# Kernel optimization log

Measured on AMD Instinct MI355X. Metric: run time of the kernel, lower is better.

The kernel has to match this reference:

```python
import jax, jax.numpy as jnp
import numpy as np

E, D, H1, H2, O, B = 100, 2048, 512, 256, 1, 1024


def setup_inputs() -> dict:
    key = jax.random.key(0)
    ks = jax.random.split(key, 7)
    s = lambda k, shape, fan_in: jax.random.normal(k, shape, jnp.float32) * (1.0 / np.sqrt(fan_in))
    return {
        "x": jax.random.normal(ks[0], (B, D), jnp.float32),
        "W1": s(ks[1], (E, D, H1), D),
        "b1": jnp.zeros((E, H1), jnp.float32),
        "W2": s(ks[2], (E, H1, H2), H1),
        "b2": jnp.zeros((E, H2), jnp.float32),
        "W3": s(ks[3], (E, H2, O), H2),
        "b3": jnp.zeros((E, O), jnp.float32),
    }


def reference(x, W1, b1, W2, b2, W3, b3):
    # Ensemble of E independent 3-layer MLPs, expressed as batched GEMMs
    # over the ensemble axis (equivalent to the torch loop + stack(dim=2)).
    h = jax.nn.relu(jnp.einsum('bd,edh->ebh', x, W1) + b1[:, None, :])   # [E,B,H1]
    h = jax.nn.relu(jnp.einsum('ebh,ehk->ebk', h, W2) + b2[:, None, :])  # [E,B,H2]
    out = jnp.einsum('ebk,eko->ebo', h, W3) + b3[:, None, :]             # [E,B,O]
    # torch.stack([...], dim=2): each model output [B,O] -> [B,O,E]
    return jnp.transpose(out, (1, 2, 0))
```

## Files before the change

### kernel.cpp

```cpp
#include <hip/hip_runtime.h>
#include <hip/hip_bf16.h>
#include <cstdint>
#include <cstddef>

#define E_  100
#define D_  2048
#define H1_ 512
#define H2_ 256
#define B_  1024

typedef __bf16 bf16x8 __attribute__((ext_vector_type(8)));
typedef float  f32x4  __attribute__((ext_vector_type(4)));

typedef __attribute__((address_space(1))) void gvoid;
typedef __attribute__((address_space(3))) void lvoid;

__device__ __forceinline__ unsigned short f2bf(float f){
    union { float f; unsigned int u; } x; x.f = f;
    unsigned int r = x.u + 0x7fffu + ((x.u >> 16) & 1u);
    return (unsigned short)(r >> 16);
}
__device__ __forceinline__ float bf2f(unsigned int u){
    union { unsigned int i; float f; } x; x.i = u << 16; return x.f;
}

__global__ __launch_bounds__(256) void cvt_x_kernel(const float* __restrict__ x,
                                                    unsigned short* __restrict__ xb){
    int i = blockIdx.x * 256 + threadIdx.x;
    float4 v = ((const float4*)x)[i];
    ushort4 o;
    o.x = f2bf(v.x); o.y = f2bf(v.y); o.z = f2bf(v.z); o.w = f2bf(v.w);
    ((ushort4*)xb)[i] = o;
}

__global__ __launch_bounds__(256) void transpose_cvt_kernel(const float* __restrict__ src,
                                                            unsigned short* __restrict__ dst,
                                                            int R, int C){
    __shared__ unsigned int T[64 * 32];
    const int e  = blockIdx.z;
    const int r0 = blockIdx.y * 64, c0 = blockIdx.x * 64;
    const float* s = src + (size_t)e * R * C;
    unsigned short* d = dst + (size_t)e * R * C;
    const int t  = threadIdx.x;
    const int c4 = (t & 15) * 4;
    #pragma unroll
    for (int pass = 0; pass < 2; ++pass){
        const int rp = (t >> 4) + pass * 16;
        const int r  = rp * 2;
        const float4 va = *(const float4*)(s + (size_t)(r0 + r)     * C + c0 + c4);
        const float4 vb = *(const float4*)(s + (size_t)(r0 + r + 1) * C + c0 + c4);
        const float aa[4] = {va.x, va.y, va.z, va.w};
        const float bb[4] = {vb.x, vb.y, vb.z, vb.w};
        #pragma unroll
        for (int i = 0; i < 4; ++i){
            const int c = c4 + i;
            const unsigned int pk = (unsigned int)f2bf(aa[i]) | ((unsigned int)f2bf(bb[i]) << 16);
            T[c * 32 + (rp ^ (c & 31))] = pk;
        }
    }
    __syncthreads();
    const int c  = t >> 2;
    const int j0 = (t & 3) * 8;
    unsigned int tmp[8];
    #pragma unroll
    for (int j = 0; j < 8; ++j)
        tmp[j] = T[c * 32 + ((j0 + j) ^ (c & 31))];
    unsigned short* drow = d + (size_t)(c0 + c) * R + r0 + j0 * 2;
    ((uint4*)drow)[0] = make_uint4(tmp[0], tmp[1], tmp[2], tmp[3]);
    ((uint4*)drow)[1] = make_uint4(tmp[4], tmp[5], tmp[6], tmp[7]);
}

__global__ __launch_bounds__(256) void gemm_bt_relu(const unsigned short* __restrict__ A,
                                                    long long aEstride,
                                                    const unsigned short* __restrict__ Bt,
                                                    const float* __restrict__ bias,
                                                    unsigned short* __restrict__ Cout,
                                                    int M, int N, int K){
    __shared__ unsigned short As[128 * 32];
    __shared__ unsigned short Bs[128 * 32];
    const int e  = blockIdx.z;
    const int m0 = blockIdx.y * 128, n0 = blockIdx.x * 128;
    const int t = threadIdx.x, lane = t & 63, wid = t >> 6;
    const int wm = wid >> 1, wn = wid & 1;

    const unsigned short* Ae = A + (size_t)e * (size_t)aEstride + (size_t)m0 * K;
    const unsigned short* Be = Bt + (size_t)e * (size_t)N * K + (size_t)n0 * K;

    const int ch0 = wid * 128 + lane;
    const int r0s = ch0 >> 2, k0s = (((ch0 & 3) ^ ((ch0 >> 3) & 3)) * 8);
    const int ch1 = ch0 + 64;
    const int r1s = ch1 >> 2, k1s = (((ch1 & 3) ^ ((ch1 >> 3) & 3)) * 8);

    f32x4 acc[4][4];
    #pragma unroll
    for (int i = 0; i < 4; ++i)
        #pragma unroll
        for (int j = 0; j < 4; ++j) acc[i][j] = 0;

    const int fr  = lane & 15;
    const int fc  = lane >> 4;
    const int fsw = (fr >> 1) & 3;
    const int fo  = ((fc ^ fsw) * 8);

    for (int k0 = 0; k0 < K; k0 += 32){
        __builtin_amdgcn_global_load_lds((gvoid*)(Ae + (size_t)r0s * K + k0 + k0s),
                                         (lvoid*)(As + (wid * 2 + 0) * 512), 16, 0, 0);
        __builtin_amdgcn_global_load_lds((gvoid*)(Ae + (size_t)r1s * K + k0 + k1s),
                                         (lvoid*)(As + (wid * 2 + 1) * 512), 16, 0, 0);
        __builtin_amdgcn_global_load_lds((gvoid*)(Be + (size_t)r0s * K + k0 + k0s),
                                         (lvoid*)(Bs + (wid * 2 + 0) * 512), 16, 0, 0);
        __builtin_amdgcn_global_load_lds((gvoid*)(Be + (size_t)r1s * K + k0 + k1s),
                                         (lvoid*)(Bs + (wid * 2 + 1) * 512), 16, 0, 0);
        __syncthreads();

        bf16x8 af[4], bf[4];
        #pragma unroll
        for (int i = 0; i < 4; ++i)
            af[i] = *(const bf16x8*)(As + (wm * 64 + i * 16 + fr) * 32 + fo);
        #pragma unroll
        for (int j = 0; j < 4; ++j)
            bf[j] = *(const bf16x8*)(Bs + (wn * 64 + j * 16 + fr) * 32 + fo);
        #pragma unroll
        for (int i = 0; i < 4; ++i)
            #pragma unroll
            for (int j = 0; j < 4; ++j)
                acc[i][j] = __builtin_amdgcn_mfma_f32_16x16x32_bf16(af[i], bf[j], acc[i][j], 0, 0, 0);
        __syncthreads();
    }

    const int row0 = m0 + wm * 64, col0 = n0 + wn * 64;
    const size_t cb = (size_t)e * (size_t)M * N;
    #pragma unroll
    for (int j = 0; j < 4; ++j){
        const int col = col0 + j * 16 + (lane & 15);
        const float bv = bias[(size_t)e * N + col];
        #pragma unroll
        for (int i = 0; i < 4; ++i){
            const int rbase = row0 + i * 16 + (lane >> 4) * 4;
            #pragma unroll
            for (int r = 0; r < 4; ++r){
                float v = acc[i][j][r] + bv;
                v = fmaxf(v, 0.0f);
                Cout[cb + (size_t)(rbase + r) * N + col] = f2bf(v);
            }
        }
    }
}

__global__ __launch_bounds__(256) void layer3_kernel(const unsigned short* __restrict__ h2,
                                                     const float* __restrict__ W3,
                                                     const float* __restrict__ b3,
                                                     float* __restrict__ out){
    const int w     = blockIdx.x * 4 + (threadIdx.x >> 6);
    const int lane  = threadIdx.x & 63;
    const int rbase = w * 16;
    const int e     = rbase >> 10;
    const float4 wv = *(const float4*)(W3 + (size_t)e * H2_ + lane * 4);
    const float  bv = b3[e];
    #pragma unroll
    for (int i = 0; i < 16; ++i){
        const int r = rbase + i;
        const uint2 hv = *(const uint2*)(h2 + (size_t)r * H2_ + lane * 4);
        float sum = bf2f(hv.x & 0xffffu) * wv.x
                  + bf2f(hv.x >> 16)     * wv.y
                  + bf2f(hv.y & 0xffffu) * wv.z
                  + bf2f(hv.y >> 16)     * wv.w;
        #pragma unroll
        for (int o = 32; o > 0; o >>= 1) sum += __shfl_down(sum, o, 64);
        if (lane == 0) out[(size_t)(r & 1023) * E_ + e] = sum + bv;
    }
}

extern "C" void kernel_launch(void* const* d_in, const int* in_sizes, int n_in,
                              void* d_out, int out_size, void* d_ws, size_t ws_size,
                              hipStream_t stream){
    const float* x  = (const float*)d_in[0];
    const float* W1 = (const float*)d_in[1];
    const float* b1 = (const float*)d_in[2];
    const float* W2 = (const float*)d_in[3];
    const float* b2 = (const float*)d_in[4];
    const float* W3 = (const float*)d_in[5];
    const float* b3 = (const float*)d_in[6];
    float* out = (float*)d_out;

    char* ws = (char*)d_ws;
    const size_t szW1t = (size_t)E_ * H1_ * D_ * 2;
    const size_t szW2t = (size_t)E_ * H2_ * H1_ * 2;
    const size_t szXb  = (size_t)B_ * D_ * 2;
    unsigned short* W1t = (unsigned short*)(ws);
    unsigned short* W2t = (unsigned short*)(ws + szW1t);
    unsigned short* xb  = (unsigned short*)(ws + szW1t + szW2t);
    unsigned short* h1  = (unsigned short*)(ws + szW1t + szW2t + szXb);
    unsigned short* h2  = (unsigned short*)(ws);

    cvt_x_kernel<<<(B_ * D_) / (256 * 4), 256, 0, stream>>>(x, xb);
    transpose_cvt_kernel<<<dim3(H1_ / 64, D_ / 64, E_), 256, 0, stream>>>(W1, W1t, D_, H1_);
    transpose_cvt_kernel<<<dim3(H2_ / 64, H1_ / 64, E_), 256, 0, stream>>>(W2, W2t, H1_, H2_);
    gemm_bt_relu<<<dim3(H1_ / 128, B_ / 128, E_), 256, 0, stream>>>(xb, 0, W1t, b1, h1, B_, H1_, D_);
    gemm_bt_relu<<<dim3(H2_ / 128, B_ / 128, E_), 256, 0, stream>>>(h1, (long long)B_ * H1_, W2t, b2, h2, B_, H2_, H1_);
    layer3_kernel<<<(E_ * B_) / 64, 256, 0, stream>>>(h2, W3, b3, out);
}
```

Before: 996.6 us.

## Use 256x256 double-buffered pipelined GEMM for layer 1

Adds a new 512-thread GEMM kernel with 256x256 output tiles, 64-wide K steps and 128KB of double-buffered LDS, for the dominant first layer. Global-to-LDS loads for the next K tiles are interleaved with MFMA quadrants, separated by explicit barriers, and MFMA sections get raised wave priority. The aim is to raise arithmetic intensity per tile and hide memory latency behind compute. The cost is one block per CU from the large LDS footprint, and fewer blocks (800) to spread across the device.

```diff
diff --git a/kernel.cpp b/kernel.cpp
--- a/kernel.cpp
+++ b/kernel.cpp
@@ -147,6 +147,171 @@
     }
 }
 
+#define PH_BAR()  asm volatile("s_barrier" ::: "memory")
+#define PH_LGKM() asm volatile("s_waitcnt lgkmcnt(0)" ::: "memory")
+
+#define LOAD_A(SB, mh) do{ \
+    _Pragma("unroll") \
+    for (int i_ = 0; i_ < 4; ++i_){ \
+        const char* p_ = (SB) + aRowBase + (mh) * 16384 + i_ * 4096; \
+        a_[i_][0] = *(const bf16x8*)(p_ + coff0); \
+        a_[i_][1] = *(const bf16x8*)(p_ + coff1); \
+    } \
+}while(0)
+
+#define LOAD_B(SB, nh) do{ \
+    _Pragma("unroll") \
+    for (int j_ = 0; j_ < 2; ++j_){ \
+        const char* p_ = (SB) + bRowBase + (nh) * 16384 + j_ * 8192; \
+        b_[j_][0] = *(const bf16x8*)(p_ + coff0); \
+        b_[j_][1] = *(const bf16x8*)(p_ + coff1); \
+    } \
+}while(0)
+
+#define MFMA_Q(mh, nh) do{ \
+    __builtin_amdgcn_s_setprio(1); \
+    _Pragma("unroll") \
+    for (int i_ = 0; i_ < 4; ++i_){ \
+        _Pragma("unroll") \
+        for (int j_ = 0; j_ < 2; ++j_){ \
+            acc[(mh)*4 + i_][(nh)*2 + j_] = __builtin_amdgcn_mfma_f32_16x16x32_bf16( \
+                a_[i_][0], b_[j_][0], acc[(mh)*4 + i_][(nh)*2 + j_], 0, 0, 0); \
+            acc[(mh)*4 + i_][(nh)*2 + j_] = __builtin_amdgcn_mfma_f32_16x16x32_bf16( \
+                a_[i_][1], b_[j_][1], acc[(mh)*4 + i_][(nh)*2 + j_], 0, 0, 0); \
+        } \
+    } \
+    __builtin_amdgcn_s_setprio(0); \
+}while(0)
+
+__global__ __launch_bounds__(512) void gemm256_bt_relu(const unsigned short* __restrict__ A,
+                                                       long long aEstride,
+                                                       const unsigned short* __restrict__ Bt,
+                                                       const float* __restrict__ bias,
+                                                       unsigned short* __restrict__ Cout,
+                                                       int M, int N, int K){
+    extern __shared__ char smem[];
+    const int e  = blockIdx.z;
+    const int m0 = blockIdx.y * 256, n0 = blockIdx.x * 256;
+    const int tid = threadIdx.x, lane = tid & 63, wid = tid >> 6;
+    const int wm = wid >> 2, wn = wid & 3;
+
+    const unsigned short* Ae = A + (size_t)e * (size_t)aEstride + (size_t)m0 * K;
+    const unsigned short* Be = Bt + (size_t)e * (size_t)N * K + (size_t)n0 * K;
+
+    const int srow = lane >> 3;
+    const int sc8  = (lane & 7) ^ srow;
+
+    const int fr = lane & 15, fc = lane >> 4;
+    const int coff0 = (fc ^ (fr & 7)) << 4;
+    const int coff1 = coff0 ^ 64;
+    const int aRowBase = (wm * 16 + fr) << 7;
+    const int bRowBase = (wn * 16 + fr) << 7;
+
+    const char* sA0 = smem;
+    const char* sA1 = smem + 32768;
+    const char* sB0 = smem + 65536;
+    const char* sB1 = smem + 98304;
+
+    auto STAGE = [&](int tt, int h){
+        const int buf = tt & 1;
+        const unsigned short* g;
+        char* l;
+        if (h < 2){
+            g = Ae + (size_t)(h * 128 + wid * 16 + srow) * (size_t)K + (size_t)tt * 64 + sc8 * 8;
+            l = smem + buf * 32768 + h * 16384 + wid * 2048;
+        } else {
+            g = Be + (size_t)((h - 2) * 128 + wid * 16 + srow) * (size_t)K + (size_t)tt * 64 + sc8 * 8;
+            l = smem + 65536 + buf * 32768 + (h - 2) * 16384 + wid * 2048;
+        }
+        __builtin_amdgcn_global_load_lds((gvoid*)g, (lvoid*)l, 16, 0, 0);
+        __builtin_amdgcn_global_load_lds((gvoid*)(g + (size_t)8 * K), (lvoid*)(l + 1024), 16, 0, 0);
+    };
+
+    f32x4 acc[8][4];
+    #pragma unroll
+    for (int i = 0; i < 8; ++i)
+        #pragma unroll
+        for (int j = 0; j < 4; ++j) acc[i][j] = 0;
+
+    bf16x8 a_[4][2], b_[2][2];
+
+    const int NT = K >> 6;
+
+    STAGE(0, 0); STAGE(0, 1); STAGE(0, 2); STAGE(0, 3);
+    STAGE(1, 0); STAGE(1, 3); STAGE(1, 1);
+    asm volatile("s_waitcnt vmcnt(6)" ::: "memory");
+    PH_BAR();
+
+    #pragma unroll 1
+    for (int it = 0; it < (NT >> 1); ++it){
+        const int T  = it * 2;
+        const int t2 = (T + 2 < NT) ? T + 2 : T + 2 - NT;
+        const int t3 = (T + 3 < NT) ? T + 3 : T + 3 - NT;
+
+        LOAD_A(sA0, 0); LOAD_B(sB0, 0);
+        STAGE(T + 1, 2);
+        PH_BAR(); PH_LGKM();
+        MFMA_Q(0, 0);
+        PH_BAR();
+        LOAD_B(sB0, 1);
+        STAGE(t2, 0);
+        PH_BAR(); PH_LGKM();
+        MFMA_Q(0, 1);
+        PH_BAR();
+        LOAD_A(sA0, 1);
+        STAGE(t2, 3);
+        PH_BAR(); PH_LGKM();
+        MFMA_Q(1, 1);
+        PH_BAR();
+        LOAD_B(sB0, 0);
+        STAGE(t2, 1);
+        PH_BAR(); PH_LGKM();
+        MFMA_Q(1, 0);
+        asm volatile("s_waitcnt vmcnt(6)" ::: "memory");
+        PH_BAR();
+        LOAD_A(sA1, 0); LOAD_B(sB1, 0);
+        STAGE(t2, 2);
+        PH_BAR(); PH_LGKM();
+        MFMA_Q(0, 0);
+        PH_BAR();
+        LOAD_B(sB1, 1);
+        STAGE(t3, 0);
+        PH_BAR(); PH_LGKM();
+        MFMA_Q(0, 1);
+        PH_BAR();
+        LOAD_A(sA1, 1);
+        STAGE(t3, 3);
+        PH_BAR(); PH_LGKM();
+        MFMA_Q(1, 1);
+        PH_BAR();
+        LOAD_B(sB1, 0);
+        STAGE(t3, 1);
+        PH_BAR(); PH_LGKM();
+        MFMA_Q(1, 0);
+        asm volatile("s_waitcnt vmcnt(6)" ::: "memory");
+        PH_BAR();
+    }
+
+    asm volatile("s_waitcnt vmcnt(0)" ::: "memory");
+
+    const size_t cb = (size_t)e * (size_t)M * N;
+    #pragma unroll
+    for (int nj = 0; nj < 4; ++nj){
+        const int col = n0 + (nj * 4 + wn) * 16 + fr;
+        const float bv = bias[(size_t)e * N + col];
+        #pragma unroll
+        for (int mi = 0; mi < 8; ++mi){
+            const int rb = m0 + (mi * 2 + wm) * 16 + fc * 4;
+            #pragma unroll
+            for (int r = 0; r < 4; ++r){
+                float v = acc[mi][nj][r] + bv;
+                v = fmaxf(v, 0.0f);
+                Cout[cb + (size_t)(rb + r) * N + col] = f2bf(v);
+            }
+        }
+    }
+}
+
 __global__ __launch_bounds__(256) void layer3_kernel(const unsigned short* __restrict__ h2,
                                                      const float* __restrict__ W3,
                                                      const float* __restrict__ b3,
@@ -193,10 +358,17 @@
     unsigned short* h1  = (unsigned short*)(ws + szW1t + szW2t + szXb);
     unsigned short* h2  = (unsigned short*)(ws);
 
+    static bool smem_attr = false;
+    if (!smem_attr){
+        (void)hipFuncSetAttribute(reinterpret_cast<const void*>(gemm256_bt_relu),
+                                  hipFuncAttributeMaxDynamicSharedMemorySize, 131072);
+        smem_attr = true;
+    }
+
     cvt_x_kernel<<<(B_ * D_) / (256 * 4), 256, 0, stream>>>(x, xb);
     transpose_cvt_kernel<<<dim3(H1_ / 64, D_ / 64, E_), 256, 0, stream>>>(W1, W1t, D_, H1_);
     transpose_cvt_kernel<<<dim3(H2_ / 64, H1_ / 64, E_), 256, 0, stream>>>(W2, W2t, H1_, H2_);
-    gemm_bt_relu<<<dim3(H1_ / 128, B_ / 128, E_), 256, 0, stream>>>(xb, 0, W1t, b1, h1, B_, H1_, D_);
+    gemm256_bt_relu<<<dim3(H1_ / 256, B_ / 256, E_), 512, 131072, stream>>>(xb, 0, W1t, b1, h1, B_, H1_, D_);
     gemm_bt_relu<<<dim3(H2_ / 128, B_ / 128, E_), 256, 0, stream>>>(h1, (long long)B_ * H1_, W2t, b2, h2, B_, H2_, H1_);
     layer3_kernel<<<(E_ * B_) / 64, 256, 0, stream>>>(h2, W3, b3, out);
 }
```

Measured after the change: 941.0 us. 5.6% less time.
